# Performance work log

Hardware: AMD Instinct MI355X
Metric: run time of the kernel (lower is better)

## Reference

```python
import jax, jax.numpy as jnp
import numpy as np

B, DIM = 64, 131072


def setup_inputs() -> dict:
    key = jax.random.key(0)
    k1, k2, k3 = jax.random.split(key, 3)
    z = jax.random.normal(k1, (B, DIM), dtype=jnp.float32)
    trace_in = jax.random.normal(k2, (B, DIM), dtype=jnp.float32)
    ctrl = jax.random.normal(k3, (B, 3), dtype=jnp.float32)
    return {"z": z, "trace_in": trace_in, "ctrl": ctrl}


def reference(z, trace_in, ctrl):
    # gates: [B,1]
    store = jax.nn.sigmoid(ctrl[:, 0:1])
    retrieve = jax.nn.sigmoid(ctrl[:, 1:2])
    # clear gate only touches the internal buffer (no effect on outputs); omitted.

    # global max-abs normalization (single scalar, as in torch: z.abs().max())
    z_norm = z / (jnp.abs(z).max() + 1e-6)

    z_f = jnp.fft.fft(z_norm)          # [B,DIM] complex64
    trace_f = jnp.fft.fft(trace_in)    # [B,DIM] complex64
    new_trace_f = trace_f + z_f * store
    new_trace = jnp.fft.ifft(new_trace_f)
    read = jnp.fft.ifft(new_trace_f * jnp.conj(z_f)) * retrieve

    dummy_ptr = jnp.zeros((z.shape[0], 1), dtype=jnp.float32)
    return (read, new_trace, dummy_ptr, jnp.array(1.0, dtype=jnp.float32))
```

## Files before the change

kernel.cpp:

```cpp
#include <hip/hip_runtime.h>
#include <math.h>

#define NROW 64
#define DIM  131072

struct cf { float x, y; };
__device__ __forceinline__ cf cadd(cf a, cf b){ return {a.x+b.x, a.y+b.y}; }
__device__ __forceinline__ cf csub(cf a, cf b){ return {a.x-b.x, a.y-b.y}; }
__device__ __forceinline__ cf cmul(cf a, cf b){ return {a.x*b.x - a.y*b.y, a.x*b.y + a.y*b.x}; }
template<int SG> __device__ __forceinline__ cf muli(cf a){
  return (SG > 0) ? cf{-a.y, a.x} : cf{a.y, -a.x};
}
__device__ __forceinline__ float sigmoidf(float x){ return 1.0f/(1.0f + __expf(-x)); }

template<int SG> __device__ __forceinline__ void fft4(cf&a0, cf&a1, cf&a2, cf&a3){
  cf e0=cadd(a0,a2), e1=csub(a0,a2), o0=cadd(a1,a3), o1=csub(a1,a3);
  cf w=muli<SG>(o1);
  a0=cadd(e0,o0); a2=csub(e0,o0); a1=cadd(e1,w); a3=csub(e1,w);
}

template<int SG> __device__ __forceinline__ void fft8(cf v[8]){
  cf e0=v[0], e1=v[2], e2=v[4], e3=v[6];
  cf o0=v[1], o1=v[3], o2=v[5], o3=v[7];
  fft4<SG>(e0,e1,e2,e3); fft4<SG>(o0,o1,o2,o3);
  const float R=0.70710678118654752f;
  cf w1=cmul(o1, cf{R, (float)SG*R});
  cf w2=muli<SG>(o2);
  cf w3=cmul(o3, cf{-R, (float)SG*R});
  v[0]=cadd(e0,o0); v[4]=csub(e0,o0);
  v[1]=cadd(e1,w1); v[5]=csub(e1,w1);
  v[2]=cadd(e2,w2); v[6]=csub(e2,w2);
  v[3]=cadd(e3,w3); v[7]=csub(e3,w3);
}

template<int SG> __device__ __forceinline__ void fft16(cf v[16]){
  cf e[8], o[8];
  #pragma unroll
  for(int i=0;i<8;i++){ e[i]=v[2*i]; o[i]=v[2*i+1]; }
  fft8<SG>(e); fft8<SG>(o);
  const float C[8]={1.f,0.92387953251128674f,0.70710678118654752f,0.38268343236508977f,
                    0.f,-0.38268343236508977f,-0.70710678118654752f,-0.92387953251128674f};
  const float S[8]={0.f,0.38268343236508977f,0.70710678118654752f,0.92387953251128674f,
                    1.f,0.92387953251128674f,0.70710678118654752f,0.38268343236508977f};
  #pragma unroll
  for(int k=0;k<8;k++){
    cf w=cmul(o[k], cf{C[k], (float)SG*S[k]});
    v[k]=cadd(e[k],w); v[k+8]=csub(e[k],w);
  }
}

__global__ void k0_tail(float* __restrict__ dout, int cplx){
  int t = threadIdx.x;
  size_t base = (size_t)2*NROW*DIM*cplx;
  if(t < NROW) dout[base + t] = 0.f;
  else if(t == NROW) dout[base + NROW] = 1.0f;
}

__global__ __launch_bounds__(256) void k1_maxabs(const float* __restrict__ z, unsigned* __restrict__ dst){
  __shared__ float red[256];
  size_t i0 = (size_t)blockIdx.x*blockDim.x + threadIdx.x;
  size_t stride = (size_t)gridDim.x*blockDim.x;
  const float4* z4 = (const float4*)z;
  size_t n4 = (size_t)NROW*DIM/4;
  float m = 0.f;
  for(size_t i=i0;i<n4;i+=stride){
    float4 v=z4[i];
    m = fmaxf(m, fmaxf(fmaxf(fabsf(v.x),fabsf(v.y)), fmaxf(fabsf(v.z),fabsf(v.w))));
  }
  red[threadIdx.x]=m; __syncthreads();
  #pragma unroll
  for(int s=128;s>0;s>>=1){
    if(threadIdx.x<(unsigned)s) red[threadIdx.x]=fmaxf(red[threadIdx.x],red[threadIdx.x+s]);
    __syncthreads();
  }
  if(threadIdx.x==0) atomicMax(dst, __float_as_uint(red[0]));
}

__global__ __launch_bounds__(256) void k2_fwd1(
    const float* __restrict__ z, const float* __restrict__ tr,
    const float* __restrict__ ctrl, const unsigned* __restrict__ maxbits,
    float2* __restrict__ Bws, float* __restrict__ out_nt, int cplx)
{
  __shared__ float reb[4384], imb[4384];
  __shared__ float twc[256], tws[256];
  int t = threadIdx.x;
  int b = blockIdx.x >> 5;
  int n1b = (blockIdx.x & 31) << 4;
  {
    float sv, cv;
    __sincosf(-0.0245436926061703f * (float)t, &sv, &cv);
    twc[t]=cv; tws[t]=sv;
  }
  float s = 1.0f/(__uint_as_float(*maxbits) + 1e-6f);
  float gs = sigmoidf(ctrl[b*3+0]);
  const float* zr  = z  + (size_t)b*DIM;
  const float* trr = tr + (size_t)b*DIM;
  #pragma unroll
  for(int it=0; it<16; ++it){
    int e = t + 256*it;
    int n2 = e >> 4, i = e & 15;
    int n = n2*512 + n1b + i;
    float zv = zr[n], tv = trr[n];
    reb[n2*17+i] = zv; imb[n2*17+i] = tv;
    float nt = fmaf(gs*s, zv, tv);
    size_t oidx = (size_t)b*DIM + n;
    if(cplx == 2) ((float2*)out_nt)[oidx] = make_float2(nt, 0.f);
    else out_nt[oidx] = nt;
  }
  __syncthreads();
  int f = t & 15, p = t >> 4;
  cf v[16];
  #pragma unroll
  for(int q=0;q<16;q++){ int n2=q*16+p; v[q].x=reb[n2*17+f]; v[q].y=imb[n2*17+f]; }
  fft16<-1>(v);
  #pragma unroll
  for(int kq=1;kq<16;kq++){ int tt=(p*kq)&255; v[kq]=cmul(v[kq], cf{twc[tt], tws[tt]}); }
  __syncthreads();
  #pragma unroll
  for(int kq=0;kq<16;kq++){ reb[f*274 + kq*17 + p]=v[kq].x; imb[f*274 + kq*17 + p]=v[kq].y; }
  __syncthreads();
  #pragma unroll
  for(int pp=0;pp<16;pp++){ v[pp].x=reb[f*274 + p*17 + pp]; v[pp].y=imb[f*274 + p*17 + pp]; }
  fft16<-1>(v);
  int nn1 = n1b + f;
  #pragma unroll
  for(int kp=0;kp<16;kp++){
    int k2 = kp*16 + p;
    int tt = (nn1*k2) & (DIM-1);
    float tf = (float)(tt - ((tt >= (DIM/2)) ? DIM : 0));
    float sv, cv;
    __sincosf(-4.793689960382698e-05f * tf, &sv, &cv);
    cf r = cmul(v[kp], cf{cv, sv});
    Bws[((size_t)b<<17) + (size_t)k2*512 + nn1] = make_float2(r.x, r.y);
  }
}

template<int SG>
__device__ __forceinline__ void fft512_block(
    float* Xre, float* Xim, float* Tre, float* Tim,
    int lane, const float* twc, const float* tws)
{
  cf v[8];
  #pragma unroll
  for(int q=0;q<8;q++){ v[q].x=Xre[q*64+lane]; v[q].y=Xim[q*64+lane]; }
  fft8<SG>(v);
  #pragma unroll
  for(int kq=1;kq<8;kq++){ int tt=(lane*kq)&511; v[kq]=cmul(v[kq], cf{twc[tt], (float)SG*tws[tt]}); }
  #pragma unroll
  for(int kq=0;kq<8;kq++){ Tre[lane*9+kq]=v[kq].x; Tim[lane*9+kq]=v[kq].y; }
  __syncthreads();
  int kQ = lane>>3, pp = lane&7;
  #pragma unroll
  for(int q=0;q<8;q++){ int idx=(q*8+pp)*9+kQ; v[q].x=Tre[idx]; v[q].y=Tim[idx]; }
  fft8<SG>(v);
  #pragma unroll
  for(int kq=1;kq<8;kq++){ int tt=(pp*kq*8)&511; v[kq]=cmul(v[kq], cf{twc[tt], (float)SG*tws[tt]}); }
  __syncthreads();
  #pragma unroll
  for(int kq=0;kq<8;kq++){ Xre[pp*73+kq*9+kQ]=v[kq].x; Xim[pp*73+kq*9+kQ]=v[kq].y; }
  __syncthreads();
  #pragma unroll
  for(int p2=0;p2<8;p2++){ int idx=p2*73 + kQ*9 + pp; v[p2].x=Xre[idx]; v[p2].y=Xim[idx]; }
  fft8<SG>(v);
  #pragma unroll
  for(int kp=0;kp<8;kp++){ int k=kp*64 + kQ*8 + pp; Tre[k]=v[kp].x; Tim[k]=v[kp].y; }
}

__global__ __launch_bounds__(128) void k3_mid(
    float2* __restrict__ Bws, const float* __restrict__ ctrl,
    const unsigned* __restrict__ maxbits)
{
  __shared__ float Xs[4*584], Ts[4*584];
  __shared__ float twc[512], tws[512];
  int t = threadIdx.x;
  int b  = blockIdx.x >> 7;
  int pr = blockIdx.x & 127;
  int cA = (pr==0) ? 0   : pr;
  int cB = (pr==0) ? 128 : 256-pr;
  int col = t >> 6, lane = t & 63;
  int myc = col ? cB : cA;
  for(int i=t;i<512;i+=128){
    float sv,cv; __sincosf(0.0122718463030851f*(float)i, &sv, &cv);
    twc[i]=cv; tws[i]=sv;
  }
  float s = 1.0f/(__uint_as_float(*maxbits)+1e-6f);
  float gs = sigmoidf(ctrl[b*3+0]);
  float alpha = sigmoidf(ctrl[b*3+1]) * (1.0f/(float)DIM);
  float* Xre = Xs + (2*col)*584; float* Xim = Xre + 584;
  float* Tre = Ts + (2*col)*584; float* Tim = Tre + 584;
  float2* colp = Bws + ((size_t)b<<17) + ((size_t)myc<<9);
  #pragma unroll
  for(int r=0;r<8;r++){ float2 vv = colp[lane + 64*r]; Xre[lane+64*r]=vv.x; Xim[lane+64*r]=vv.y; }
  __syncthreads();
  fft512_block<-1>(Xre, Xim, Tre, Tim, lane, twc, tws);
  __syncthreads();
  const float* Pre = (pr==0) ? Tre : (Ts + (2*(1-col))*584);
  const float* Pim = Pre + 584;
  #pragma unroll
  for(int r=0;r<8;r++){
    int k1  = lane + 64*r;
    int k1p = (myc==0) ? ((512-k1)&511) : (511-k1);
    float cr = Tre[k1], ci = Tim[k1];
    float qr = Pre[k1p], qi = -Pim[k1p];
    float zur = 0.5f*(cr+qr), zui = 0.5f*(ci+qi);
    float dr = cr-qr, di = ci-qi;
    float tfr = 0.5f*di, tfi = -0.5f*dr;
    float szr = s*zur, szi = s*zui;
    float ntr = fmaf(gs, szr, tfr), nti = fmaf(gs, szi, tfi);
    float prr = (ntr*szr + nti*szi)*alpha;
    float pii = (nti*szr - ntr*szi)*alpha;
    Xre[k1]=prr; Xim[k1]=pii;
  }
  __syncthreads();
  fft512_block<1>(Xre, Xim, Tre, Tim, lane, twc, tws);
  __syncthreads();
  #pragma unroll
  for(int r=0;r<8;r++){
    int m1 = lane + 64*r;
    int tt = (m1*myc) & (DIM-1);
    float tf = (float)(tt - ((tt>=(DIM/2))?DIM:0));
    float sv,cv; __sincosf(4.793689960382698e-05f*tf, &sv, &cv);
    cf r2 = cmul(cf{Tre[m1],Tim[m1]}, cf{cv,sv});
    colp[m1] = make_float2(r2.x, r2.y);
  }
}

__global__ __launch_bounds__(256) void k4_inv2(
    const float2* __restrict__ Qws, float* __restrict__ dout, int cplx)
{
  __shared__ float reb[4384], imb[4384];
  __shared__ float twc[256], tws[256];
  int t = threadIdx.x;
  int b = blockIdx.x >> 5;
  int m1b = (blockIdx.x & 31) << 4;
  {
    float sv, cv;
    __sincosf(0.0245436926061703f * (float)t, &sv, &cv);
    twc[t]=cv; tws[t]=sv;
  }
  #pragma unroll
  for(int it=0; it<16; ++it){
    int e = t + 256*it;
    int k2 = e >> 4, i = e & 15;
    float2 q = Qws[((size_t)b<<17) + (size_t)k2*512 + m1b + i];
    reb[k2*17+i]=q.x; imb[k2*17+i]=q.y;
  }
  __syncthreads();
  int f = t & 15, p = t >> 4;
  cf v[16];
  #pragma unroll
  for(int q=0;q<16;q++){ int k2=q*16+p; v[q].x=reb[k2*17+f]; v[q].y=imb[k2*17+f]; }
  fft16<1>(v);
  #pragma unroll
  for(int kq=1;kq<16;kq++){ int tt=(p*kq)&255; v[kq]=cmul(v[kq], cf{twc[tt], tws[tt]}); }
  __syncthreads();
  #pragma unroll
  for(int kq=0;kq<16;kq++){ reb[f*274+kq*17+p]=v[kq].x; imb[f*274+kq*17+p]=v[kq].y; }
  __syncthreads();
  #pragma unroll
  for(int pp=0;pp<16;pp++){ v[pp].x=reb[f*274+p*17+pp]; v[pp].y=imb[f*274+p*17+pp]; }
  fft16<1>(v);
  #pragma unroll
  for(int kp=0;kp<16;kp++){
    int m2 = kp*16 + p;
    size_t n = (size_t)(m1b + f) + (size_t)512*m2;
    size_t oidx = (size_t)b*DIM + n;
    if(cplx==2) ((float2*)dout)[oidx] = make_float2(v[kp].x, 0.f);
    else dout[oidx] = v[kp].x;
  }
}

extern "C" void kernel_launch(void* const* d_in, const int* in_sizes, int n_in,
                              void* d_out, int out_size, void* d_ws, size_t ws_size,
                              hipStream_t stream)
{
  (void)in_sizes; (void)n_in; (void)ws_size;
  const float* z    = (const float*)d_in[0];
  const float* tr   = (const float*)d_in[1];
  const float* ctrl = (const float*)d_in[2];
  float* dout = (float*)d_out;
  int cplx = (out_size > 20000000) ? 2 : 1;
  unsigned* maxbits = (unsigned*)d_ws;
  float2* Bws = (float2*)((char*)d_ws + 256);

  hipMemsetAsync(d_ws, 0, 4, stream);
  hipLaunchKernelGGL(k0_tail,  dim3(1),    dim3(128), 0, stream, dout, cplx);
  hipLaunchKernelGGL(k1_maxabs,dim3(256),  dim3(256), 0, stream, z, maxbits);
  hipLaunchKernelGGL(k2_fwd1,  dim3(2048), dim3(256), 0, stream,
                     z, tr, ctrl, maxbits, Bws, dout + (size_t)NROW*DIM*cplx, cplx);
  hipLaunchKernelGGL(k3_mid,   dim3(8192), dim3(128), 0, stream, Bws, ctrl, maxbits);
  hipLaunchKernelGGL(k4_inv2,  dim3(2048), dim3(256), 0, stream, Bws, dout, cplx);
}
```

Measured before the change: 212.7 us.

## Vectorize loads and stores, use nontemporal writes, replace per-element sincos with twiddle recurrence

```diff
diff --git a/kernel.cpp b/kernel.cpp
--- a/kernel.cpp
+++ b/kernel.cpp
@@ -12,6 +12,9 @@
   return (SG > 0) ? cf{-a.y, a.x} : cf{a.y, -a.x};
 }
 __device__ __forceinline__ float sigmoidf(float x){ return 1.0f/(1.0f + __expf(-x)); }
+
+typedef float __attribute__((ext_vector_type(4))) fvec4;
+typedef float __attribute__((ext_vector_type(2))) fvec2;
 
 template<int SG> __device__ __forceinline__ void fft4(cf&a0, cf&a1, cf&a2, cf&a3){
   cf e0=cadd(a0,a2), e1=csub(a0,a2), o0=cadd(a1,a3), o1=csub(a1,a3);
@@ -93,19 +96,34 @@
   }
   float s = 1.0f/(__uint_as_float(*maxbits) + 1e-6f);
   float gs = sigmoidf(ctrl[b*3+0]);
-  const float* zr  = z  + (size_t)b*DIM;
-  const float* trr = tr + (size_t)b*DIM;
-  #pragma unroll
-  for(int it=0; it<16; ++it){
+  float cc = gs*s;
+  const float4* zr4 = (const float4*)(z  + (size_t)b*DIM);
+  const float4* tr4 = (const float4*)(tr + (size_t)b*DIM);
+  #pragma unroll
+  for(int it=0; it<4; ++it){
     int e = t + 256*it;
-    int n2 = e >> 4, i = e & 15;
-    int n = n2*512 + n1b + i;
-    float zv = zr[n], tv = trr[n];
-    reb[n2*17+i] = zv; imb[n2*17+i] = tv;
-    float nt = fmaf(gs*s, zv, tv);
+    int n2 = e >> 2, j4 = e & 3;
+    int fi = n2*128 + (n1b>>2) + j4;
+    float4 zv = zr4[fi];
+    float4 tv = tr4[fi];
+    int lb = n2*17 + j4*4;
+    reb[lb+0]=zv.x; reb[lb+1]=zv.y; reb[lb+2]=zv.z; reb[lb+3]=zv.w;
+    imb[lb+0]=tv.x; imb[lb+1]=tv.y; imb[lb+2]=tv.z; imb[lb+3]=tv.w;
+    float n0 = fmaf(cc, zv.x, tv.x);
+    float n1v= fmaf(cc, zv.y, tv.y);
+    float n2v= fmaf(cc, zv.z, tv.z);
+    float n3 = fmaf(cc, zv.w, tv.w);
+    size_t n = (size_t)n2*512 + n1b + j4*4;
     size_t oidx = (size_t)b*DIM + n;
-    if(cplx == 2) ((float2*)out_nt)[oidx] = make_float2(nt, 0.f);
-    else out_nt[oidx] = nt;
+    if(cplx == 2){
+      fvec4 a  = {n0, 0.f, n1v, 0.f};
+      fvec4 bq = {n2v, 0.f, n3, 0.f};
+      fvec4* op = (fvec4*)((float2*)out_nt + oidx);
+      __builtin_nontemporal_store(a,  op);
+      __builtin_nontemporal_store(bq, op+1);
+    } else {
+      out_nt[oidx+0]=n0; out_nt[oidx+1]=n1v; out_nt[oidx+2]=n2v; out_nt[oidx+3]=n3;
+    }
   }
   __syncthreads();
   int f = t & 15, p = t >> 4;
@@ -123,15 +141,20 @@
   for(int pp=0;pp<16;pp++){ v[pp].x=reb[f*274 + p*17 + pp]; v[pp].y=imb[f*274 + p*17 + pp]; }
   fft16<-1>(v);
   int nn1 = n1b + f;
+  cf w, st;
+  {
+    float sv, cv;
+    __sincosf(-4.793689960382698e-05f * (float)(nn1*p), &sv, &cv);
+    w = {cv, sv};
+    __sincosf(-4.793689960382698e-05f * 16.f * (float)nn1, &sv, &cv);
+    st = {cv, sv};
+  }
   #pragma unroll
   for(int kp=0;kp<16;kp++){
     int k2 = kp*16 + p;
-    int tt = (nn1*k2) & (DIM-1);
-    float tf = (float)(tt - ((tt >= (DIM/2)) ? DIM : 0));
-    float sv, cv;
-    __sincosf(-4.793689960382698e-05f * tf, &sv, &cv);
-    cf r = cmul(v[kp], cf{cv, sv});
+    cf r = cmul(v[kp], w);
     Bws[((size_t)b<<17) + (size_t)k2*512 + nn1] = make_float2(r.x, r.y);
+    w = cmul(w, st);
   }
 }
 
@@ -214,14 +237,20 @@
   __syncthreads();
   fft512_block<1>(Xre, Xim, Tre, Tim, lane, twc, tws);
   __syncthreads();
+  cf w, st;
+  {
+    float sv,cv;
+    __sincosf(4.793689960382698e-05f * (float)(lane*myc), &sv, &cv);
+    w = {cv, sv};
+    __sincosf(4.793689960382698e-05f * 64.f * (float)myc, &sv, &cv);
+    st = {cv, sv};
+  }
   #pragma unroll
   for(int r=0;r<8;r++){
     int m1 = lane + 64*r;
-    int tt = (m1*myc) & (DIM-1);
-    float tf = (float)(tt - ((tt>=(DIM/2))?DIM:0));
-    float sv,cv; __sincosf(4.793689960382698e-05f*tf, &sv, &cv);
-    cf r2 = cmul(cf{Tre[m1],Tim[m1]}, cf{cv,sv});
+    cf r2 = cmul(cf{Tre[m1],Tim[m1]}, w);
     colp[m1] = make_float2(r2.x, r2.y);
+    w = cmul(w, st);
   }
 }
 
@@ -238,12 +267,15 @@
     __sincosf(0.0245436926061703f * (float)t, &sv, &cv);
     twc[t]=cv; tws[t]=sv;
   }
-  #pragma unroll
-  for(int it=0; it<16; ++it){
+  const float4* Qp = (const float4*)(Qws + ((size_t)b<<17));
+  #pragma unroll
+  for(int it=0; it<8; ++it){
     int e = t + 256*it;
-    int k2 = e >> 4, i = e & 15;
-    float2 q = Qws[((size_t)b<<17) + (size_t)k2*512 + m1b + i];
-    reb[k2*17+i]=q.x; imb[k2*17+i]=q.y;
+    int k2 = e >> 3, j = e & 7;
+    float4 q = Qp[k2*256 + (m1b>>1) + j];
+    int lb = k2*17 + 2*j;
+    reb[lb+0]=q.x; imb[lb+0]=q.y;
+    reb[lb+1]=q.z; imb[lb+1]=q.w;
   }
   __syncthreads();
   int f = t & 15, p = t >> 4;
@@ -265,7 +297,10 @@
     int m2 = kp*16 + p;
     size_t n = (size_t)(m1b + f) + (size_t)512*m2;
     size_t oidx = (size_t)b*DIM + n;
-    if(cplx==2) ((float2*)dout)[oidx] = make_float2(v[kp].x, 0.f);
+    if(cplx==2){
+      fvec2 rv = {v[kp].x, 0.f};
+      __builtin_nontemporal_store(rv, (fvec2*)((float2*)dout + oidx));
+    }
     else dout[oidx] = v[kp].x;
   }
 }
@@ -285,7 +320,7 @@
 
   hipMemsetAsync(d_ws, 0, 4, stream);
   hipLaunchKernelGGL(k0_tail,  dim3(1),    dim3(128), 0, stream, dout, cplx);
-  hipLaunchKernelGGL(k1_maxabs,dim3(256),  dim3(256), 0, stream, z, maxbits);
+  hipLaunchKernelGGL(k1_maxabs,dim3(1024), dim3(256), 0, stream, z, maxbits);
   hipLaunchKernelGGL(k2_fwd1,  dim3(2048), dim3(256), 0, stream,
                      z, tr, ctrl, maxbits, Bws, dout + (size_t)NROW*DIM*cplx, cplx);
   hipLaunchKernelGGL(k3_mid,   dim3(8192), dim3(128), 0, stream, Bws, ctrl, maxbits);
```

Measured after the change: 218.7 us. +2.8%, slower.
